# Kernel optimization log

Measured on AMD Instinct MI355X. Metric: run time of the kernel, lower is better.

## Reference

```python
import jax, jax.numpy as jnp
import numpy as np

N, K, M0, M1, RB = 8192, 16, 128, 64, 42
RCUT = 32.0
KSEQ_HALF = 8  # source hardcodes k_seqnn = 16 -> half-band of 8


def knn(coord, mask, k):
    # O(n^2) distance matrix + top_k, with sequence-band forcing (k_seq is not None path)
    n = coord.shape[0]
    d2 = jnp.sum(jnp.square(coord[:, None, :] - coord[None, :, :]), axis=-1)  # [n,n]
    mm = mask[:, None] & mask[None, :]
    d2 = jnp.where(mm, d2, jnp.inf)
    idx = jnp.arange(n)
    dd = jnp.abs(idx[:, None] - idx[None, :])
    band = (dd >= 1) & (dd <= KSEQ_HALF)          # equals the roll/triu/tril loop in source
    d2 = jnp.where(band & mm, -jnp.inf, d2)       # force sequence neighbors first
    d2 = jnp.where(idx[:, None] == idx[None, :], jnp.inf, d2)
    neg, nei = jax.lax.top_k(-d2, k + 1)
    return nei[:, 1:], neg[:, 1:] != -jnp.inf


def setup_inputs() -> dict:
    key = jax.random.key(0)
    ks = jax.random.split(key, 10)
    return {
        "coord": jax.random.normal(ks[0], (N, 3), jnp.float32) * 5.0,
        "feat_s": jax.random.normal(ks[1], (N, M0), jnp.float32),
        "feat_v": jax.random.normal(ks[2], (N, M1, 3), jnp.float32),
        "mask": jnp.ones((N,), dtype=bool),
        "W0": jax.random.normal(ks[3], (M0 + M1 + 1, M0), jnp.float32),   # 193 -> 128 scalar linear
        "W1": jax.random.normal(ks[4], (M1 + M0 + M1 + 1, M1), jnp.float32),  # 257 -> 64 vector linear
        "mlp_w1": jax.random.normal(ks[5], (M0 + RB + M0, RB), jnp.float32),  # 298 -> 42
        "mlp_b1": jnp.zeros((RB,), jnp.float32),
        "mlp_w2": jax.random.normal(ks[6], (RB, M0 + M1), jnp.float32),       # 42 -> 192 (num_irreps)
        "mlp_b2": jnp.zeros((M0 + M1,), jnp.float32),
        "w_move": jax.random.normal(ks[7], (M1,), jnp.float32),
    }


def reference(coord, feat_s, feat_v, mask, W0, W1, mlp_w1, mlp_b1, mlp_w2, mlp_b2, w_move):
    nei, nmask = knn(coord, mask, K)                       # [n,k] int, [n,k] bool
    nm = nmask[:, :, None].astype(coord.dtype)             # [n,k,1]
    vectors = coord[nei] - coord[:, None, :]               # [n,k,3]
    norm2 = jnp.sum(vectors ** 2, axis=-1)
    norm = jnp.sqrt(jnp.where(norm2 == 0.0, 1.0, norm2))   # [n,k]
    # spherical harmonics, edge_irreps = 0e + 1e, normalize=False, component norm
    sh0 = nm[..., 0]                                       # [n,k]  (1 * mask)
    sh1 = nm * jnp.sqrt(3.0) * vectors                     # [n,k,3]
    # soft_one_hot_linspace, fourier basis, cutoff=True
    x = (norm / RCUT)[..., None]
    i = jnp.arange(1, RB + 1, dtype=coord.dtype)
    rad = jnp.where((x > 0.0) & (x < 1.0),
                    jnp.sin(jnp.pi * i * x) / jnp.sqrt(0.25 + RB / 2), 0.0) * nm  # [n,k,RB]
    # gather neighbor features
    ns = nm * feat_s[nei]                                  # [n,k,M0]
    nv = nm[..., None] * feat_v[nei]                       # [n,k,M1,3]
    # tensor products (0e+1e) x (M0x0e + M1x1e); 1x1->2e paths are dropped by the
    # output Linear (irreps_out has no 2e), so they are not computed.
    tp_s_a = sh0[..., None] * ns                                        # 0e x 0e -> [n,k,M0]
    tp_s_b = jnp.einsum('nki,nkci->nkc', sh1, nv) / jnp.sqrt(3.0)       # 1e x 1e -> 0e [n,k,M1]
    tp_v_a = sh0[..., None, None] * nv                                  # 0e x 1e [n,k,M1,3]
    tp_v_b = sh1[:, :, None, :] * ns[..., None]                         # 1e x 0e [n,k,M0,3]
    tp_v_c = jnp.cross(jnp.broadcast_to(sh1[:, :, None, :], nv.shape), nv) / jnp.sqrt(2.0)  # 1x1->1e
    in_s = jnp.concatenate([tp_s_a, tp_s_b, sh0[..., None]], axis=-1)               # [n,k,193]
    in_v = jnp.concatenate([tp_v_a, tp_v_b, tp_v_c, sh1[:, :, None, :]], axis=-2)   # [n,k,257,3]
    # e3nn Linear: per-l dense mix with 1/sqrt(fan_in)
    msg_s = jnp.einsum('nkc,cd->nkd', in_s, W0) / jnp.sqrt(1.0 * in_s.shape[-1])    # [n,k,M0]
    msg_v = jnp.einsum('nkci,cd->nkdi', in_v, W1) / jnp.sqrt(1.0 * in_v.shape[-2])  # [n,k,M1,3]
    # MLP mix over scalar channels: [msg 0e | rad | node 0e broadcast]
    feat_s_exp = jnp.broadcast_to(feat_s[:, None, :], (N, K, M0))
    mix_in = jnp.concatenate([msg_s, rad, feat_s_exp], axis=-1)                      # [n,k,298]
    h = jax.nn.silu(mix_in @ mlp_w1 / jnp.sqrt(1.0 * mix_in.shape[-1]) + mlp_b1)
    mix = h @ mlp_w2 / jnp.sqrt(1.0 * RB) + mlp_b2                                   # [n,k,192]
    mix_s, mix_v = mix[..., :M0], mix[..., M0:]
    # gate per irrep and aggregate over neighbors
    out_s = jnp.sum(msg_s * mix_s, axis=1) / K                                       # [n,M0]
    out_v = jnp.sum(msg_v * mix_v[..., None], axis=1) / K                            # [n,M1,3]
    # move: 0.001 * Linear('1e')
    new_coord = coord + 0.001 * jnp.einsum('nci,c->ni', out_v, w_move) / jnp.sqrt(1.0 * M1)
    # Residual on irreps_array (norm=False)
    return feat_s + out_s, feat_v + out_v, new_coord
```

## Files before the change

kernel.cpp:

```cpp
#include <hip/hip_runtime.h>
#include <math.h>

namespace {

typedef unsigned short u16;
typedef short bf16x8 __attribute__((ext_vector_type(8)));
typedef float f32x4 __attribute__((ext_vector_type(4)));
typedef unsigned short u16x4 __attribute__((ext_vector_type(4)));
typedef unsigned short u16x2 __attribute__((ext_vector_type(2)));

constexpr int NPTS = 8192;
constexpr int KNB  = 16;

constexpr int OFF_W0   = 0;
constexpr int OFF_PH2  = 25600;
constexpr int P2_WM1   = 0;
constexpr int P2_WM1E  = 9600;
constexpr int P2_W1A   = 16128;
constexpr int P2_W1C   = 20736;
constexpr int PH2_SZ   = 25344;
constexpr int OFF_W1B  = 50944;
constexpr int OFF_WM2  = 59648;
constexpr int WCOPY    = 73472;
constexpr int NCOPY    = 8;

__device__ __forceinline__ u16 f2bf(float f) {
  return (u16)((__float_as_uint(f) + 0x8000u) >> 16);
}
__device__ __forceinline__ unsigned int pk2bf(float a, float b) {
  const unsigned int ua = __float_as_uint(a) + 0x8000u;
  const unsigned int ub = __float_as_uint(b) + 0x8000u;
  return __builtin_amdgcn_perm(ub, ua, 0x07060302);
}

__device__ __forceinline__ void wave_argmin(float& best, int& bj) {
#pragma unroll
  for (int off = 32; off; off >>= 1) {
    float ob = __shfl_xor(best, off);
    int   oj = __shfl_xor(bj, off);
    if (ob < best || (ob == best && oj < bj)) { best = ob; bj = oj; }
  }
}

__global__ __launch_bounds__(256) void setup_all(
    const float* __restrict__ coord,
    const float* __restrict__ W0, const float* __restrict__ W1,
    const float* __restrict__ w1, const float* __restrict__ w2,
    u16* __restrict__ Wrep, float* __restrict__ w0last, float* __restrict__ w1last,
    int* __restrict__ nei) {
  const int b = blockIdx.x;
  if (b < 288) {
    const int t = b * 256 + threadIdx.x;
    if (t < WCOPY) {
      u16 val = 0;
      int i = t;
      if (i < 25600)                 { const int d = i/200, c = i%200; if (c < 192) val = f2bf(W0[c*128 + d]); }
      else if ((i -= 25600) < 9600)  { const int r = i/200, c = i%200; if (r < 42 && c < 170) val = f2bf(w1[c*42 + r]); }
      else if ((i -= 9600)  < 6528)  { const int r = i/136, c = i%136; if (r < 42 && c < 128) val = f2bf(w1[(170+c)*42 + r]); }
      else if ((i -= 6528)  < 4608)  { const int d = i/72,  c = i%72;  if (c < 64)  val = f2bf(W1[c*64 + d]); }
      else if ((i -= 4608)  < 4608)  { const int d = i/72,  c = i%72;  if (c < 64)  val = f2bf(W1[(192+c)*64 + d]); }
      else if ((i -= 4608)  < 8704)  { const int d = i/136, c = i%136; if (c < 128) val = f2bf(W1[(64+c)*64 + d]); }
      else { i -= 8704;                const int e = i/72,  rr = i%72; if (rr < 42) val = f2bf(w2[rr*192 + e]); }
#pragma unroll
      for (int cp = 0; cp < NCOPY; ++cp) Wrep[cp*WCOPY + t] = val;
      return;
    }
    int t2 = t - WCOPY;
    if (t2 < 128) { w0last[t2] = W0[192*128 + t2]; return; }
    t2 -= 128;
    if (t2 < 64)  { w1last[t2] = W1[256*64 + t2]; return; }
    return;
  }
  if (b < 800) {
    const int lane = threadIdx.x & 63;
    const int wid  = (b - 288) * 4 + (threadIdx.x >> 6);
    int p[4]; float cx[4], cy[4], cz[4], best[4]; int bj[4];
#pragma unroll
    for (int t = 0; t < 4; ++t) {
      p[t] = wid + 2048 * t;
      cx[t] = coord[3*p[t]+0]; cy[t] = coord[3*p[t]+1]; cz[t] = coord[3*p[t]+2];
      best[t] = 3.0e38f; bj[t] = NPTS;
    }
    for (int j = lane; j < NPTS; j += 64) {
      const float x = coord[3*j+0], y = coord[3*j+1], z = coord[3*j+2];
#pragma unroll
      for (int t = 0; t < 4; ++t) {
        int dd = j - p[t]; dd = dd < 0 ? -dd : dd;
        const float dx = x-cx[t], dy = y-cy[t], dz = z-cz[t];
        const float d2 = dx*dx + dy*dy + dz*dz;
        if (dd > 8 && d2 < best[t]) { best[t] = d2; bj[t] = j; }
      }
    }
#pragma unroll
    for (int t = 0; t < 4; ++t) {
      wave_argmin(best[t], bj[t]);
      const int pp = p[t];
      if (pp >= 8 && pp < NPTS-8) {
        if (lane < 15) nei[pp*KNB + lane] = pp - 7 + lane + (lane >= 7 ? 1 : 0);
        if (lane == 15) nei[pp*KNB + 15] = bj[t];
      }
    }
    return;
  }
  {
    const int eb = b - 800;
    const int n = (eb < 8) ? eb : (NPTS - 16 + eb);
    const int tid = threadIdx.x;
    const int lane = tid & 63;
    const int wv = tid >> 6;
    __shared__ float l_best[4];
    __shared__ int   l_bj[4];
    __shared__ int   l_sel;
    __shared__ int   s_sel[9];
    const float cx = coord[3*n+0], cy = coord[3*n+1], cz = coord[3*n+2];
    float d2v[32];
    unsigned int alive = 0;
#pragma unroll
    for (int q = 0; q < 32; ++q) {
      const int j = tid + q * 256;
      int dd = j - n; dd = dd < 0 ? -dd : dd;
      const float dx = coord[3*j+0]-cx, dy = coord[3*j+1]-cy, dz = coord[3*j+2]-cz;
      d2v[q] = dx*dx + dy*dy + dz*dz;
      if (dd > 8) alive |= (1u << q);
    }
    const int lo = (n-8 < 0) ? 0 : n-8;
    const int hi = (n+8 > NPTS-1) ? NPTS-1 : n+8;
    const int s  = (KNB + 1) - (hi - lo);
    for (int p = 0; p < s; ++p) {
      float best = 3.0e38f; int bj = NPTS;
#pragma unroll
      for (int q = 0; q < 32; ++q) {
        if ((alive >> q) & 1u) {
          const int j = tid + q * 256;
          if (d2v[q] < best) { best = d2v[q]; bj = j; }
        }
      }
      wave_argmin(best, bj);
      if (lane == 0) { l_best[wv] = best; l_bj[wv] = bj; }
      __syncthreads();
      if (tid == 0) {
        float bb = l_best[0]; int jj = l_bj[0];
        for (int w2 = 1; w2 < 4; ++w2)
          if (l_best[w2] < bb || (l_best[w2] == bb && l_bj[w2] < jj)) { bb = l_best[w2]; jj = l_bj[w2]; }
        l_sel = jj; s_sel[p] = jj;
      }
      __syncthreads();
      const int dq = l_sel - tid;
      if (dq >= 0 && (dq & 255) == 0) alive &= ~(1u << (dq >> 8));
      __syncthreads();
    }
    if (tid == 0) {
      const int first = (lo == n) ? (lo + 1) : lo;
      int idx = 0;
      for (int j = lo; j <= hi; ++j) {
        if (j == n || j == first) continue;
        nei[n*KNB + (idx++)] = j;
      }
      for (int p = 0; p < s; ++p) nei[n*KNB + (idx++)] = s_sel[p];
    }
  }
}

__device__ __forceinline__ void stage(u16* dst, const u16* src, int n, int t) {
  for (int i = t*8; i < n; i += 4096)
    __builtin_amdgcn_global_load_lds(
        (const __attribute__((address_space(1))) unsigned int*)(src + i),
        (__attribute__((address_space(3))) unsigned int*)(dst + i), 16, 0, 0);
}

#define LFRAG(BUF, ldk, cb, kb) (*(const bf16x8*)&(BUF)[((cb)*16 + colb)*(ldk) + (kb)*32 + rowg*8])

__global__ __launch_bounds__(512, 2) void conv_mfma(
    const float* __restrict__ coord,
    const float* __restrict__ feat_s,
    const float* __restrict__ feat_v,
    const int*   __restrict__ nei,
    const u16*   __restrict__ Wrep,
    const float* __restrict__ w0last,
    const float* __restrict__ w1last,
    const float* __restrict__ b1,
    const float* __restrict__ b2,
    const float* __restrict__ w_move,
    float* __restrict__ out) {

  __shared__ __align__(16) u16 wbuf[25600];
  __shared__ __align__(16) u16 wbuf2[13824];
  __shared__ __align__(16) u16 bA[16][16][136];
  __shared__ float s_vec[16][16][4];
  __shared__ int   s_nei[16][16];

  const int t = threadIdx.x;
  const int w = t >> 6;
  const int l = t & 63;
  const int colb = l & 15;
  const int rowg = l >> 4;
  const int nb = blockIdx.x * 16;
  const int p0 = nb + 2*w;
  const u16* Wc = Wrep + (blockIdx.x & 7) * WCOPY;

  constexpr float RS193 = 0.07198158f;
  constexpr float RS257 = 0.06237829f;
  constexpr float RS298 = 0.05792841f;
  constexpr float RS42  = 0.15430335f;
  constexpr float IS2   = 0.70710678f;
  constexpr float SQ3   = 1.73205081f;
  constexpr float RINV  = 0.21693046f;

  stage(wbuf,  Wc + OFF_W0,  25600, t);
  stage(wbuf2, Wc + OFF_W1B, 8704,  t);

  union U8 { unsigned int d[4]; u16 u[8]; bf16x8 v; };
  bf16x8 aS[2][4], aT[2][2];

#pragma unroll
  for (int m = 0; m < 2; ++m) {
    const int pt = 2*w + m;
    const int pm = p0 + m;
    if (l < 16) {
      const int j = nei[pm*KNB + l];
      s_nei[pt][l] = j;
      const float v0 = coord[3*j+0] - coord[3*pm+0];
      const float v1 = coord[3*j+1] - coord[3*pm+1];
      const float v2 = coord[3*j+2] - coord[3*pm+2];
      const float n2 = v0*v0 + v1*v1 + v2*v2;
      s_vec[pt][l][0] = v0; s_vec[pt][l][1] = v1; s_vec[pt][l][2] = v2;
      s_vec[pt][l][3] = sqrtf(n2 == 0.0f ? 1.0f : n2);
    }
    const int jn = s_nei[pt][colb];
    const float v0 = s_vec[pt][colb][0], v1 = s_vec[pt][colb][1], v2 = s_vec[pt][colb][2];
    const float* fsp = feat_s + jn*128 + rowg*8;
#pragma unroll
    for (int kb = 0; kb < 4; ++kb) {
      const float4 a = *(const float4*)(fsp + kb*32);
      const float4 b = *(const float4*)(fsp + kb*32 + 4);
      U8 tt;
      tt.d[0] = pk2bf(a.x, a.y); tt.d[1] = pk2bf(a.z, a.w);
      tt.d[2] = pk2bf(b.x, b.y); tt.d[3] = pk2bf(b.z, b.w);
      aS[m][kb] = tt.v;
    }
    const float* fvp = feat_v + jn*192 + rowg*24;
#pragma unroll
    for (int kv = 0; kv < 2; ++kv) {
      float f[24];
#pragma unroll
      for (int q = 0; q < 6; ++q)
        *(float4*)&f[q*4] = *(const float4*)(fvp + kv*96 + q*4);
      U8 tt;
#pragma unroll
      for (int e = 0; e < 8; e += 2) {
        tt.d[e>>1] = pk2bf(f[e*3+0]*v0 + f[e*3+1]*v1 + f[e*3+2]*v2,
                           f[e*3+3]*v0 + f[e*3+4]*v1 + f[e*3+5]*v2);
      }
      aT[m][kv] = tt.v;
    }
  }
  __syncthreads();

  float msgs[2][8][4];
  {
    f32x4 accS[2][8];
#pragma unroll
    for (int m = 0; m < 2; ++m)
#pragma unroll
      for (int cb = 0; cb < 8; ++cb) accS[m][cb] = (f32x4){0.f,0.f,0.f,0.f};
#pragma unroll
    for (int kb = 0; kb < 6; ++kb) {
      bf16x8 bw[8];
#pragma unroll
      for (int cb = 0; cb < 8; ++cb) bw[cb] = LFRAG(wbuf, 200, cb, kb);
#pragma unroll
      for (int m = 0; m < 2; ++m) {
        const bf16x8 aF = (kb < 4) ? aS[m][kb] : aT[m][kb-4];
#pragma unroll
        for (int cb = 0; cb < 8; ++cb)
          accS[m][cb] = __builtin_amdgcn_mfma_f32_16x16x32_bf16(aF, bw[cb], accS[m][cb], 0, 0, 0);
      }
    }
#pragma unroll
    for (int m = 0; m < 2; ++m)
#pragma unroll
      for (int cb = 0; cb < 8; ++cb) {
        const int col = cb*16 + colb;
        const float w0l = w0last[col];
#pragma unroll
        for (int jj = 0; jj < 4; ++jj) {
          const float v = (accS[m][cb][jj] + w0l) * RS193;
          msgs[m][cb][jj] = v;
          bA[2*w+m][rowg*4 + jj][col] = f2bf(v);
        }
      }
  }

  f32x4 accB[2][4];
#pragma unroll
  for (int m = 0; m < 2; ++m)
#pragma unroll
    for (int cb = 0; cb < 4; ++cb) accB[m][cb] = (f32x4){0.f,0.f,0.f,0.f};
#pragma unroll
  for (int kb = 0; kb < 4; ++kb) {
    bf16x8 bw[4];
#pragma unroll
    for (int cb = 0; cb < 4; ++cb) bw[cb] = LFRAG(wbuf2, 136, cb, kb);
#pragma unroll
    for (int m = 0; m < 2; ++m)
#pragma unroll
      for (int cb = 0; cb < 4; ++cb)
        accB[m][cb] = __builtin_amdgcn_mfma_f32_16x16x32_bf16(aS[m][kb], bw[cb], accB[m][cb], 0, 0, 0);
  }

  __syncthreads();
  stage(wbuf,  Wc + OFF_PH2, PH2_SZ, t);
  stage(wbuf2, Wc + OFF_WM2, 13824,  t);
  __syncthreads();

  {
    f32x4 accH[2][3];
#pragma unroll
    for (int m = 0; m < 2; ++m)
#pragma unroll
      for (int cb = 0; cb < 3; ++cb) accH[m][cb] = (f32x4){0.f,0.f,0.f,0.f};
#pragma unroll
    for (int kb = 0; kb < 4; ++kb) {
      bf16x8 bw[3];
#pragma unroll
      for (int cb = 0; cb < 3; ++cb) bw[cb] = LFRAG(wbuf + P2_WM1, 200, cb, kb);
#pragma unroll
      for (int m = 0; m < 2; ++m) {
        const bf16x8 aF = *(const bf16x8*)&bA[2*w+m][colb][kb*32 + rowg*8];
#pragma unroll
        for (int cb = 0; cb < 3; ++cb)
          accH[m][cb] = __builtin_amdgcn_mfma_f32_16x16x32_bf16(aF, bw[cb], accH[m][cb], 0, 0, 0);
      }
    }
    bf16x8 radF[2][2];
#pragma unroll
    for (int m = 0; m < 2; ++m) {
      const float x = s_vec[2*w+m][colb][3] * (1.0f/32.0f);
      U8 r0, r1;
#pragma unroll
      for (int e = 0; e < 8; ++e) {
        const int ch0 = rowg*8 + e;
        const int ch1 = 32 + rowg*8 + e;
        const float s0 = (x < 1.0f) ? __sinf(3.14159265f*(float)(ch0+1)*x) * RINV : 0.0f;
        const float s1 = (ch1 < 42 && x < 1.0f) ? __sinf(3.14159265f*(float)(ch1+1)*x) * RINV : 0.0f;
        r0.u[e] = f2bf(s0); r1.u[e] = f2bf(s1);
      }
      radF[m][0] = r0.v; radF[m][1] = r1.v;
    }
#pragma unroll
    for (int kb = 4; kb < 6; ++kb) {
      bf16x8 bw[3];
#pragma unroll
      for (int cb = 0; cb < 3; ++cb) bw[cb] = LFRAG(wbuf + P2_WM1, 200, cb, kb);
#pragma unroll
      for (int m = 0; m < 2; ++m)
#pragma unroll
        for (int cb = 0; cb < 3; ++cb)
          accH[m][cb] = __builtin_amdgcn_mfma_f32_16x16x32_bf16(radF[m][kb-4], bw[cb], accH[m][cb], 0, 0, 0);
    }
#pragma unroll
    for (int kb = 0; kb < 4; ++kb) {
      bf16x8 bw[3];
#pragma unroll
      for (int cb = 0; cb < 3; ++cb) bw[cb] = LFRAG(wbuf + P2_WM1E, 136, cb, kb);
#pragma unroll
      for (int m = 0; m < 2; ++m) {
        const float* fcp = feat_s + (p0+m)*128 + rowg*8;
        const float4 a = *(const float4*)(fcp + kb*32);
        const float4 b = *(const float4*)(fcp + kb*32 + 4);
        U8 tt;
        tt.d[0] = pk2bf(a.x, a.y); tt.d[1] = pk2bf(a.z, a.w);
        tt.d[2] = pk2bf(b.x, b.y); tt.d[3] = pk2bf(b.z, b.w);
#pragma unroll
        for (int cb = 0; cb < 3; ++cb)
          accH[m][cb] = __builtin_amdgcn_mfma_f32_16x16x32_bf16(tt.v, bw[cb], accH[m][cb], 0, 0, 0);
      }
    }
#pragma unroll
    for (int m = 0; m < 2; ++m) {
#pragma unroll
      for (int cb = 0; cb < 3; ++cb) {
        const int rr = cb*16 + colb;
        const float bv = (rr < 42) ? b1[rr] : 0.f;
#pragma unroll
        for (int jj = 0; jj < 4; ++jj) {
          float hv = 0.f;
          if (rr < 42) {
            const float z = accH[m][cb][jj] * RS298 + bv;
            hv = z / (1.0f + __expf(-z));
          }
          bA[2*w+m][rowg*4 + jj][rr] = f2bf(hv);
        }
      }
      *(u16x4*)&bA[2*w+m][colb][48 + rowg*4] = (u16x4){0,0,0,0};
    }
  }

  {
    f32x4 accM[2][8];
#pragma unroll
    for (int m = 0; m < 2; ++m)
#pragma unroll
      for (int cb = 0; cb < 8; ++cb) accM[m][cb] = (f32x4){0.f,0.f,0.f,0.f};
#pragma unroll
    for (int kb = 0; kb < 2; ++kb) {
      bf16x8 bw[8];
#pragma unroll
      for (int cb = 0; cb < 8; ++cb) bw[cb] = LFRAG(wbuf2, 72, cb, kb);
#pragma unroll
      for (int m = 0; m < 2; ++m) {
        const bf16x8 aF = *(const bf16x8*)&bA[2*w+m][colb][kb*32 + rowg*8];
#pragma unroll
        for (int cb = 0; cb < 8; ++cb)
          accM[m][cb] = __builtin_amdgcn_mfma_f32_16x16x32_bf16(aF, bw[cb], accM[m][cb], 0, 0, 0);
      }
    }
#pragma unroll
    for (int m = 0; m < 2; ++m) {
      const int pm = p0 + m;
      float s_lo = 0.f, s_hi = 0.f;
#pragma unroll
      for (int cb = 0; cb < 8; ++cb) {
        const int col = cb*16 + colb;
        const float b2v = b2[col];
        float s = 0.f;
#pragma unroll
        for (int jj = 0; jj < 4; ++jj)
          s += msgs[m][cb][jj] * (accM[m][cb][jj] * RS42 + b2v);
        s += __shfl_xor(s, 16);
        s += __shfl_xor(s, 32);
        if (cb == rowg)     s_lo = s;
        if (cb == rowg + 4) s_hi = s;
      }
      out[pm*128 + l]      = feat_s[pm*128 + l]      + s_lo * 0.0625f;
      out[pm*128 + 64 + l] = feat_s[pm*128 + 64 + l] + s_hi * 0.0625f;
    }
  }

  f32x4 accMv[2][4];
#pragma unroll
  for (int m = 0; m < 2; ++m)
#pragma unroll
    for (int cb = 0; cb < 4; ++cb) accMv[m][cb] = (f32x4){0.f,0.f,0.f,0.f};
#pragma unroll
  for (int kb = 0; kb < 2; ++kb) {
    bf16x8 bw[4];
#pragma unroll
    for (int cb = 0; cb < 4; ++cb) bw[cb] = LFRAG(wbuf2, 72, cb + 8, kb);
#pragma unroll
    for (int m = 0; m < 2; ++m) {
      const bf16x8 aF = *(const bf16x8*)&bA[2*w+m][colb][kb*32 + rowg*8];
#pragma unroll
      for (int cb = 0; cb < 4; ++cb)
        accMv[m][cb] = __builtin_amdgcn_mfma_f32_16x16x32_bf16(aF, bw[cb], accMv[m][cb], 0, 0, 0);
    }
  }

  bf16x8 aV0[2][2], aV1[2][2], aV2[2][2];
#pragma unroll
  for (int m = 0; m < 2; ++m) {
    const int pt = 2*w + m;
    const int jn = s_nei[pt][colb];
    const float* fvp = feat_v + jn*192 + rowg*24;
#pragma unroll
    for (int kv = 0; kv < 2; ++kv) {
      float f[24];
#pragma unroll
      for (int q = 0; q < 6; ++q)
        *(float4*)&f[q*4] = *(const float4*)(fvp + kv*96 + q*4);
      U8 t0, t1, t2;
#pragma unroll
      for (int e = 0; e < 8; e += 2) {
        t0.d[e>>1] = pk2bf(f[e*3+0], f[e*3+3]);
        t1.d[e>>1] = pk2bf(f[e*3+1], f[e*3+4]);
        t2.d[e>>1] = pk2bf(f[e*3+2], f[e*3+5]);
      }
      aV0[m][kv] = t0.v; aV1[m][kv] = t1.v; aV2[m][kv] = t2.v;
    }
  }
  float sh[2][4][3];
#pragma unroll
  for (int m = 0; m < 2; ++m)
#pragma unroll
    for (int jj = 0; jj < 4; ++jj) {
      const int rr = rowg*4 + jj;
      sh[m][jj][0] = SQ3 * s_vec[2*w+m][rr][0];
      sh[m][jj][1] = SQ3 * s_vec[2*w+m][rr][1];
      sh[m][jj][2] = SQ3 * s_vec[2*w+m][rr][2];
    }
  float ov0[2] = {0.f,0.f}, ov1[2] = {0.f,0.f}, ov2[2] = {0.f,0.f};
#pragma unroll
  for (int cb = 0; cb < 4; ++cb) {
    f32x4 aA0[2], aA1[2], aA2[2], aC0[2], aC1[2], aC2[2];
#pragma unroll
    for (int m = 0; m < 2; ++m) {
      aA0[m] = (f32x4){0.f,0.f,0.f,0.f}; aA1[m] = (f32x4){0.f,0.f,0.f,0.f}; aA2[m] = (f32x4){0.f,0.f,0.f,0.f};
      aC0[m] = (f32x4){0.f,0.f,0.f,0.f}; aC1[m] = (f32x4){0.f,0.f,0.f,0.f}; aC2[m] = (f32x4){0.f,0.f,0.f,0.f};
    }
#pragma unroll
    for (int kv = 0; kv < 2; ++kv) {
      const bf16x8 ba = LFRAG(wbuf + P2_W1A, 72, cb, kv);
      const bf16x8 bc = LFRAG(wbuf + P2_W1C, 72, cb, kv);
#pragma unroll
      for (int m = 0; m < 2; ++m) {
        aA0[m] = __builtin_amdgcn_mfma_f32_16x16x32_bf16(aV0[m][kv], ba, aA0[m], 0, 0, 0);
        aA1[m] = __builtin_amdgcn_mfma_f32_16x16x32_bf16(aV1[m][kv], ba, aA1[m], 0, 0, 0);
        aA2[m] = __builtin_amdgcn_mfma_f32_16x16x32_bf16(aV2[m][kv], ba, aA2[m], 0, 0, 0);
        aC0[m] = __builtin_amdgcn_mfma_f32_16x16x32_bf16(aV0[m][kv], bc, aC0[m], 0, 0, 0);
        aC1[m] = __builtin_amdgcn_mfma_f32_16x16x32_bf16(aV1[m][kv], bc, aC1[m], 0, 0, 0);
        aC2[m] = __builtin_amdgcn_mfma_f32_16x16x32_bf16(aV2[m][kv], bc, aC2[m], 0, 0, 0);
      }
    }
    const int d = cb*16 + colb;
    const float wl = w1last[d];
    const float b2v = b2[128 + d];
#pragma unroll
    for (int m = 0; m < 2; ++m) {
      float sv0 = 0.f, sv1 = 0.f, sv2 = 0.f;
#pragma unroll
      for (int jj = 0; jj < 4; ++jj) {
        const float bb = accB[m][cb][jj] + wl;
        const float h0 = sh[m][jj][0], h1 = sh[m][jj][1], h2 = sh[m][jj][2];
        const float m0 = (aA0[m][jj] + h0*bb + (h1*aC2[m][jj] - h2*aC1[m][jj])*IS2) * RS257;
        const float m1 = (aA1[m][jj] + h1*bb + (h2*aC0[m][jj] - h0*aC2[m][jj])*IS2) * RS257;
        const float m2 = (aA2[m][jj] + h2*bb + (h0*aC1[m][jj] - h1*aC0[m][jj])*IS2) * RS257;
        const float mx = accMv[m][cb][jj] * RS42 + b2v;
        sv0 += m0 * mx; sv1 += m1 * mx; sv2 += m2 * mx;
      }
      sv0 += __shfl_xor(sv0, 16); sv0 += __shfl_xor(sv0, 32);
      sv1 += __shfl_xor(sv1, 16); sv1 += __shfl_xor(sv1, 32);
      sv2 += __shfl_xor(sv2, 16); sv2 += __shfl_xor(sv2, 32);
      if (cb == rowg) { ov0[m] = sv0 * 0.0625f; ov1[m] = sv1 * 0.0625f; ov2[m] = sv2 * 0.0625f; }
    }
  }

#pragma unroll
  for (int m = 0; m < 2; ++m) {
    const int pm = p0 + m;
    const int vb = pm*192 + l*3;
    out[NPTS*128 + vb + 0] = feat_v[vb + 0] + ov0[m];
    out[NPTS*128 + vb + 1] = feat_v[vb + 1] + ov1[m];
    out[NPTS*128 + vb + 2] = feat_v[vb + 2] + ov2[m];
    const float wm = w_move[l];
    float cn0 = ov0[m] * wm, cn1 = ov1[m] * wm, cn2 = ov2[m] * wm;
#pragma unroll
    for (int off = 1; off <= 32; off <<= 1) {
      cn0 += __shfl_xor(cn0, off);
      cn1 += __shfl_xor(cn1, off);
      cn2 += __shfl_xor(cn2, off);
    }
    if (l == 0) {
      const int oc = NPTS*(128+192) + pm*3;
      out[oc+0] = coord[pm*3+0] + 1.25e-4f * cn0;
      out[oc+1] = coord[pm*3+1] + 1.25e-4f * cn1;
      out[oc+2] = coord[pm*3+2] + 1.25e-4f * cn2;
    }
  }
}

}

extern "C" void kernel_launch(void* const* d_in, const int* in_sizes, int n_in,
                              void* d_out, int out_size, void* d_ws, size_t ws_size,
                              hipStream_t stream) {
  const float* coord  = (const float*)d_in[0];
  const float* feat_s = (const float*)d_in[1];
  const float* feat_v = (const float*)d_in[2];
  const float* W0     = (const float*)d_in[4];
  const float* W1     = (const float*)d_in[5];
  const float* w1     = (const float*)d_in[6];
  const float* b1     = (const float*)d_in[7];
  const float* w2     = (const float*)d_in[8];
  const float* b2     = (const float*)d_in[9];
  const float* wmove  = (const float*)d_in[10];
  float* out = (float*)d_out;

  char* ws = (char*)d_ws;
  int*   nei    = (int*)  (ws + 0);
  u16*   Wrep   = (u16*)  (ws + 524288);
  float* w0last = (float*)(ws + 1699840);
  float* w1last = (float*)(ws + 1700352);

  setup_all<<<816, 256, 0, stream>>>(coord, W0, W1, w1, w2, Wrep, w0last, w1last, nei);
  conv_mfma<<<NPTS/16, 512, 0, stream>>>(coord, feat_s, feat_v, nei, Wrep,
                                         w0last, w1last, b1, b2, wmove, out);
}
```

Before: 111.1 us.

## Split kNN candidate scan across four blocks and merge with packed atomicMin

The brute-force nearest-non-band-neighbor search is split so that each group of query points is scanned by four blocks, each covering a quarter of the candidates. The partial results are merged through a 64-bit atomicMin on packed (distance bits, index). Band neighbors are no longer written to the neighbor array; the conv kernel computes them from the point index and reads the 16th neighbor from the packed word. This trades an extra memset launch and atomics for four times more parallelism in the setup kernel's scan phase, which previously ran on only 512 blocks.

```diff
diff --git a/kernel.cpp b/kernel.cpp
--- a/kernel.cpp
+++ b/kernel.cpp
@@ -8,6 +8,7 @@
 typedef float f32x4 __attribute__((ext_vector_type(4)));
 typedef unsigned short u16x4 __attribute__((ext_vector_type(4)));
 typedef unsigned short u16x2 __attribute__((ext_vector_type(2)));
+typedef unsigned long long u64;
 
 constexpr int NPTS = 8192;
 constexpr int KNB  = 16;
@@ -47,7 +48,7 @@
     const float* __restrict__ W0, const float* __restrict__ W1,
     const float* __restrict__ w1, const float* __restrict__ w2,
     u16* __restrict__ Wrep, float* __restrict__ w0last, float* __restrict__ w1last,
-    int* __restrict__ nei) {
+    int* __restrict__ nei, u64* __restrict__ packed) {
   const int b = blockIdx.x;
   if (b < 288) {
     const int t = b * 256 + threadIdx.x;
@@ -71,9 +72,12 @@
     if (t2 < 64)  { w1last[t2] = W1[256*64 + t2]; return; }
     return;
   }
-  if (b < 800) {
+  if (b < 2336) {
+    const int qb = b - 288;
+    const int g  = qb >> 2;
+    const int q  = qb & 3;
     const int lane = threadIdx.x & 63;
-    const int wid  = (b - 288) * 4 + (threadIdx.x >> 6);
+    const int wid  = g * 4 + (threadIdx.x >> 6);
     int p[4]; float cx[4], cy[4], cz[4], best[4]; int bj[4];
 #pragma unroll
     for (int t = 0; t < 4; ++t) {
@@ -81,7 +85,8 @@
       cx[t] = coord[3*p[t]+0]; cy[t] = coord[3*p[t]+1]; cz[t] = coord[3*p[t]+2];
       best[t] = 3.0e38f; bj[t] = NPTS;
     }
-    for (int j = lane; j < NPTS; j += 64) {
+    const int j0 = q * 2048;
+    for (int j = j0 + lane; j < j0 + 2048; j += 64) {
       const float x = coord[3*j+0], y = coord[3*j+1], z = coord[3*j+2];
 #pragma unroll
       for (int t = 0; t < 4; ++t) {
@@ -95,15 +100,13 @@
     for (int t = 0; t < 4; ++t) {
       wave_argmin(best[t], bj[t]);
       const int pp = p[t];
-      if (pp >= 8 && pp < NPTS-8) {
-        if (lane < 15) nei[pp*KNB + lane] = pp - 7 + lane + (lane >= 7 ? 1 : 0);
-        if (lane == 15) nei[pp*KNB + 15] = bj[t];
-      }
+      if (lane == 0 && pp >= 8 && pp < NPTS-8)
+        atomicMin(&packed[pp], ((u64)__float_as_uint(best[t]) << 32) | (unsigned)bj[t]);
     }
     return;
   }
   {
-    const int eb = b - 800;
+    const int eb = b - 2336;
     const int n = (eb < 8) ? eb : (NPTS - 16 + eb);
     const int tid = threadIdx.x;
     const int lane = tid & 63;
@@ -175,6 +178,7 @@
     const float* __restrict__ feat_s,
     const float* __restrict__ feat_v,
     const int*   __restrict__ nei,
+    const u64*   __restrict__ packed,
     const u16*   __restrict__ Wrep,
     const float* __restrict__ w0last,
     const float* __restrict__ w1last,
@@ -217,7 +221,15 @@
     const int pt = 2*w + m;
     const int pm = p0 + m;
     if (l < 16) {
-      const int j = nei[pm*KNB + l];
+      int j;
+      const bool is_edge = (pm < 8) || (pm >= NPTS-8);
+      if (is_edge) {
+        j = nei[pm*KNB + l];
+      } else if (l < 15) {
+        j = pm - 7 + l + (l >= 7 ? 1 : 0);
+      } else {
+        j = (int)(unsigned)(packed[pm] & 0xFFFFFFFFull);
+      }
       s_nei[pt][l] = j;
       const float v0 = coord[3*j+0] - coord[3*pm+0];
       const float v1 = coord[3*j+1] - coord[3*pm+1];
@@ -580,8 +592,11 @@
   u16*   Wrep   = (u16*)  (ws + 524288);
   float* w0last = (float*)(ws + 1699840);
   float* w1last = (float*)(ws + 1700352);
-
-  setup_all<<<816, 256, 0, stream>>>(coord, W0, W1, w1, w2, Wrep, w0last, w1last, nei);
-  conv_mfma<<<NPTS/16, 512, 0, stream>>>(coord, feat_s, feat_v, nei, Wrep,
+  u64*   packed = (u64*)  (ws + 1700608);
+
+  hipMemsetAsync(packed, 0xFF, NPTS * sizeof(u64), stream);
+  setup_all<<<2352, 256, 0, stream>>>(coord, W0, W1, w1, w2, Wrep, w0last, w1last,
+                                      nei, packed);
+  conv_mfma<<<NPTS/16, 512, 0, stream>>>(coord, feat_s, feat_v, nei, packed, Wrep,
                                          w0last, w1last, b1, b2, wmove, out);
 }
```

Measured after the change: 106.6 us. 4.1% less time.
